# Performance work log

Measured on AMD Instinct MI355X. Metric: run time of the kernel, lower is better.

The kernel has to match this reference:

```python
import jax, jax.numpy as jnp
import numpy as np
from jax import lax

H = 1024  # hidden_size
L = 2     # num_layers


def gru_cell(x, h, Wih, Whh, bih, bhh):
    # PyTorch GRU gate order: r, z, n
    gi = x @ Wih.T + bih          # [B, 3H]
    gh = h @ Whh.T + bhh          # [B, 3H]
    ir, iz, inn = jnp.split(gi, 3, axis=-1)
    hr, hz, hn = jnp.split(gh, 3, axis=-1)
    r = jax.nn.sigmoid(ir + hr)
    z = jax.nn.sigmoid(iz + hz)
    n = jnp.tanh(inn + r * hn)
    return (1.0 - z) * n + z * h


def stacked_step(h, x_t, layers):
    # h: [L, B, H]; x_t: [B, in]; layers: list of (Wih, Whh, bih, bhh)
    hs = []
    inp = x_t
    for l, (Wih, Whh, bih, bhh) in enumerate(layers):
        hl = gru_cell(inp, h[l], Wih, Whh, bih, bhh)
        hs.append(hl)
        inp = hl
    return jnp.stack(hs), inp  # new hidden stack, top-layer output


def run_gru_seq(x_seq, h0, layers):
    # x_seq: [B, S, in] -> scan over time
    def step(h, x_t):
        h_new, out = stacked_step(h, x_t, layers)
        return h_new, out
    h_final, outs = lax.scan(step, h0, jnp.transpose(x_seq, (1, 0, 2)))
    return outs[-1], h_final  # last-timestep top-layer output [B, H]


def setup_inputs() -> dict:
    key = jax.random.key(0)
    ks = jax.random.split(key, 10)
    B, S = 128, 256

    def xavier(k, shape):
        fan_out, fan_in = shape
        std = np.sqrt(2.0 / (fan_in + fan_out))
        return jax.random.normal(k, shape, dtype=jnp.float32) * std

    inp = {
        "x": jax.random.normal(ks[0], (B, S), dtype=jnp.float32),
        "h0": jax.random.uniform(ks[1], (L, B, H), dtype=jnp.float32) * 0.01,
        "Wih0": xavier(ks[2], (3 * H, 1)),
        "Whh0": xavier(ks[3], (3 * H, H)),
        "bih0": jnp.zeros((3 * H,), jnp.float32),
        "bhh0": jnp.zeros((3 * H,), jnp.float32),
        "Wih1": xavier(ks[4], (3 * H, H)),
        "Whh1": xavier(ks[5], (3 * H, H)),
        "bih1": jnp.zeros((3 * H,), jnp.float32),
        "bhh1": jnp.zeros((3 * H,), jnp.float32),
        "fc_w": jax.random.uniform(ks[6], (1, H), jnp.float32, -1.0 / np.sqrt(H), 1.0 / np.sqrt(H)),
        "fc_b": jax.random.uniform(ks[7], (1,), jnp.float32, -1.0 / np.sqrt(H), 1.0 / np.sqrt(H)),
        "forcast_length": 8,
    }
    return inp


def reference(x, h0, Wih0, Whh0, bih0, bhh0, Wih1, Whh1, bih1, bhh1, fc_w, fc_b, forcast_length):
    layers = [(Wih0, Whh0, bih0, bhh0), (Wih1, Whh1, bih1, bhh1)]

    # forecast step i=0: full conditioning sequence
    out0, h = run_gru_seq(x[..., None], h0, layers)   # [B, H], [L, B, H]
    y0 = out0 @ fc_w.T + fc_b                          # [B, 1]

    def fstep(carry, _):
        xc, hc = carry                                 # xc: [B, 1]
        h_new, out = stacked_step(hc, xc, layers)
        y = out @ fc_w.T + fc_b                        # [B, 1]
        return (y, h_new), y[:, 0]

    (y_last, h_final), ys = lax.scan(fstep, (y0, h), None, length=forcast_length - 1)
    forcast_out = jnp.concatenate([y0[:, 0][None, :], ys], axis=0)  # [F, B]
    return jnp.mean(forcast_out, axis=0), h_final
```

## Files before the change

kernel.cpp:

```cpp
#include <hip/hip_runtime.h>

#define NB 128
#define NH 1024
#define NS 256
#define NF 8
#define NBLK 192
#define NTH 512
#define AG  __HIP_MEMORY_SCOPE_AGENT

#define GLOBL 0
#define RELL  64
#define INITL 128
#define XCNT  192
#define XARR  512
#define XCPY  1024

typedef _Float16 half_t;
typedef _Float16 f16x8 __attribute__((ext_vector_type(8)));
typedef float f32x4 __attribute__((ext_vector_type(4)));
typedef unsigned long long u64;

struct GP {
    const float *x, *hin, *Wih0, *Whh0, *bih0, *bhh0, *Wih1, *Whh1, *bih1, *bhh1, *fcw, *fcb;
    float *ypart, *out;
    half_t *h0b0, *h0b1, *h1b0, *h1b1;
    char *reg;
    unsigned *bar;
};

__device__ __forceinline__ float fast_sigmoid(float x) { return 1.0f / (1.0f + __expf(-x)); }
__device__ __forceinline__ float fast_tanh(float x) {
    float e = __expf(2.0f * x);
    return (e - 1.0f) / (e + 1.0f);
}

__device__ __forceinline__ u64 ldu64(const void* p) {
    return __hip_atomic_load((const u64*)p, __ATOMIC_RELAXED, AG);
}
__device__ __forceinline__ void stu64(void* p, u64 v) {
    __hip_atomic_store((u64*)p, v, __ATOMIC_RELAXED, AG);
}
__device__ __forceinline__ float ldf32(const float* p) {
    return __hip_atomic_load(p, __ATOMIC_RELAXED, AG);
}
__device__ __forceinline__ void stf32(float* p, float v) {
    __hip_atomic_store(p, v, __ATOMIC_RELAXED, AG);
}
__device__ __forceinline__ unsigned aadd(unsigned* p, unsigned v) {
    return __hip_atomic_fetch_add(p, v, __ATOMIC_RELAXED, AG);
}
__device__ __forceinline__ unsigned ald(const unsigned* p) {
    return __hip_atomic_load(p, __ATOMIC_RELAXED, AG);
}

__device__ __forceinline__ void l2add(unsigned* p, unsigned v) {
    asm volatile("global_atomic_add %0, %1, off" :: "v"(p), "v"(v) : "memory");
}
__device__ __forceinline__ unsigned l2add_rtn(unsigned* p, unsigned v) {
    unsigned ret;
    asm volatile("global_atomic_add %0, %1, %2, off sc0\n\ts_waitcnt vmcnt(0)"
                 : "=v"(ret) : "v"(p), "v"(v) : "memory");
    return ret;
}

__global__ void k_init(const float* __restrict__ hin, half_t* __restrict__ h0h,
                       half_t* __restrict__ h1h) {
    int i = blockIdx.x * 256 + threadIdx.x;
    h0h[i] = (half_t)hin[i];
    h1h[i] = (half_t)hin[NB * NH + i];
}

__global__ __launch_bounds__(NTH)
void k_gru(GP p) {
    extern __shared__ char lds[];
    const int tid = threadIdx.x;
    const int l   = tid & 63;
    const int wv  = tid >> 6;
    const int bid = blockIdx.x;
    const int role = (bid < 64) ? 0 : 1;
    const int lc   = bid - 64;
    const int colbase = role ? lc * 8 : bid * 16;
    float* hl  = (float*)(lds + 98304);
    int* meta  = (int*)(lds + 106496);
    unsigned* bar = p.bar;

    const int cloc = l & 15;
    const int col8 = cloc & 7;

    {
        for (int i = tid; i < 12288; i += NTH) {
            int row = i >> 8, j = i & 255;
            const float* Wsrc;
            int wrow;
            if (role == 0) {
                Wsrc = p.Whh0; wrow = (row >> 4) * NH + colbase + (row & 15);
            } else {
                int plane = row >> 3, cl = row & 7;
                Wsrc = (plane < 3) ? p.Wih1 : p.Whh1;
                int g = (plane < 3) ? plane : plane - 3;
                wrow = g * NH + colbase + cl;
            }
            float4 v = *(const float4*)(Wsrc + (size_t)wrow * NH + j * 4);
            union { half_t h[4]; uint2 u; } cv;
            cv.h[0] = (half_t)v.x; cv.h[1] = (half_t)v.y;
            cv.h[2] = (half_t)v.z; cv.h[3] = (half_t)v.w;
            *(uint2*)(lds + (row * 2048 + ((j * 8) ^ ((row & 7) << 4)))) = cv.u;
        }
        if (role == 0) {
            for (int i = tid; i < NB * 16; i += NTH)
                hl[i] = p.hin[(size_t)(i >> 4) * NH + colbase + (i & 15)];
        } else {
            for (int i = tid; i < NB * 8; i += NTH)
                hl[i] = p.hin[(size_t)NB * NH + (size_t)(i >> 3) * NH + colbase + (i & 7)];
        }
    }

    if (tid == 0) {
        unsigned x;
        asm volatile("s_getreg_b32 %0, hwreg(HW_REG_XCC_ID)" : "=s"(x));
        x &= 7;
        unsigned r = aadd(bar + XCNT + x * 32, 1u);
        asm volatile("s_waitcnt vmcnt(0)" ::: "memory");
        aadd(bar + INITL, 1u);
        while (ald(bar + INITL) < NBLK) __builtin_amdgcn_s_sleep(1);
        int nn = 0, cnt = 0;
        for (int k = 0; k < 8; ++k) {
            unsigned c = ald(bar + XCNT + k * 32);
            if (c) ++cnt;
            if (k == (int)x) nn = (int)c;
        }
        meta[0] = (int)x; meta[1] = (int)r; meta[2] = nn; meta[3] = cnt;
    }
    __syncthreads();
    const int xcd_  = meta[0];
    const int rank_ = meta[1];
    const int n_    = meta[2];
    const int nx_   = meta[3];

    float bi_[3] = {0,0,0}, bh_[3] = {0,0,0}, wx_[3] = {0,0,0}, fcwv = 0.f, fcb_ = 0.f;
    float bi_lo = 0.f, bh_lo = 0.f, bi2 = 0.f, bh2 = 0.f;
    if (role == 0) {
        int c = colbase + cloc;
        #pragma unroll
        for (int g = 0; g < 3; ++g) {
            bi_[g] = p.bih0[g * NH + c]; bh_[g] = p.bhh0[g * NH + c];
            wx_[g] = p.Wih0[g * NH + c];
        }
        fcb_ = p.fcb[0];
    } else {
        int glo = cloc >> 3;
        int c8 = colbase + col8;
        bi_lo = p.bih1[glo * NH + c8]; bh_lo = p.bhh1[glo * NH + c8];
        bi2   = p.bih1[2 * NH + c8];   bh2   = p.bhh1[2 * NH + c8];
        fcwv  = p.fcw[c8];
    }

    const int rb_l0[3] = { cloc * 2048, (16 + cloc) * 2048, (32 + cloc) * 2048 };
    const int rb_l1[4] = { cloc * 2048, (16 + col8) * 2048, (24 + cloc) * 2048, (40 + col8) * 2048 };
    const int rmask = (col8) << 4;
    const int kb0 = (l >> 4) << 4;
    const int arow = wv * 16 + cloc;
    const int b0base = wv * 16 + ((l >> 4) << 2);
    const int aloff = (l >> 4) * 2048 + arow * 16;

    auto gbar = [&](unsigned t) {
        __syncthreads();
        if (tid == 0) {
            l2add(bar + XARR + xcd_ * 32, 1u);
            if (rank_ == 0) {
                while (l2add_rtn(bar + XARR + xcd_ * 32, 0u) < (unsigned)n_ * t)
                    __builtin_amdgcn_s_sleep(1);
                unsigned old = aadd(bar + GLOBL, 1u);
                if (old == (unsigned)nx_ * t - 1u) aadd(bar + RELL, 1u);
            }
            while (ald(bar + RELL) < t) __builtin_amdgcn_s_sleep(1);
        }
        __syncthreads();
        asm volatile("buffer_inv" ::: "memory");
    };

    auto xcopy = [&](const half_t* h0s, const half_t* h1s, int slot) {
        char* dst = p.reg + ((size_t)(xcd_ * 2 + slot)) * 524288;
        for (int idx = rank_ * NTH + tid; idx < 32768; idx += n_ * NTH) {
            int which = idx >> 14, kq = (idx >> 7) & 127, row = idx & 127;
            const half_t* s = (which ? h1s : h0s) + row * 1024 + kq * 8;
            union { u64 u[2]; uint4 v; } t;
            t.u[0] = ldu64(s);
            t.u[1] = ldu64(s + 4);
            *(uint4*)(dst + which * 262144 + (size_t)(kq * 128 + row) * 16) = t.v;
        }
    };
    auto csync = [&](unsigned ct) {
        __syncthreads();
        if (tid == 0) {
            l2add(bar + XCPY + xcd_ * 32, 1u);
            while (l2add_rtn(bar + XCPY + xcd_ * 32, 0u) < (unsigned)n_ * ct)
                __builtin_amdgcn_s_sleep(1);
        }
        __syncthreads();
    };

    auto gemm_l0 = [&](const char* regA, f32x4 (&acc)[3]) {
        const char* ap = regA + aloff;
        #pragma unroll 8
        for (int ks = 0; ks < 32; ++ks) {
            f16x8 a = *(const f16x8*)(ap + (size_t)ks * 8192);
            int kb = ks * 64 + kb0;
            #pragma unroll
            for (int g = 0; g < 3; ++g) {
                f16x8 bf = *(const f16x8*)(lds + rb_l0[g] + (kb ^ rmask));
                acc[g] = __builtin_amdgcn_mfma_f32_16x16x32_f16(a, bf, acc[g], 0, 0, 0);
            }
        }
    };

    auto gemm_l1 = [&](const char* regA, f32x4 (&acc)[4]) {
        const char* ap0 = regA + aloff;
        const char* ap1 = regA + 262144 + aloff;
        #pragma unroll 8
        for (int ks = 0; ks < 32; ++ks) {
            f16x8 a0 = *(const f16x8*)(ap0 + (size_t)ks * 8192);
            f16x8 a1 = *(const f16x8*)(ap1 + (size_t)ks * 8192);
            int kb = ks * 64 + kb0;
            f16x8 b0 = *(const f16x8*)(lds + rb_l1[0] + (kb ^ rmask));
            acc[0] = __builtin_amdgcn_mfma_f32_16x16x32_f16(a0, b0, acc[0], 0, 0, 0);
            f16x8 b1 = *(const f16x8*)(lds + rb_l1[1] + (kb ^ rmask));
            acc[1] = __builtin_amdgcn_mfma_f32_16x16x32_f16(a0, b1, acc[1], 0, 0, 0);
            f16x8 b2 = *(const f16x8*)(lds + rb_l1[2] + (kb ^ rmask));
            acc[2] = __builtin_amdgcn_mfma_f32_16x16x32_f16(a1, b2, acc[2], 0, 0, 0);
            f16x8 b3 = *(const f16x8*)(lds + rb_l1[3] + (kb ^ rmask));
            acc[3] = __builtin_amdgcn_mfma_f32_16x16x32_f16(a1, b3, acc[3], 0, 0, 0);
        }
    };

    auto pack_store16 = [&](half_t* hw, int b, float hn) {
        unsigned v = (unsigned)__builtin_bit_cast(unsigned short, (half_t)hn);
        unsigned o = __shfl_xor(v, 1);
        unsigned pair = (l & 1) ? (o | (v << 16)) : (v | (o << 16));
        unsigned p2 = __shfl_xor(pair, 2);
        u64 quad = (l & 2) ? (((u64)pair << 32) | p2) : ((u64)pair | ((u64)p2 << 32));
        if ((l & 3) == 0) stu64(hw + (size_t)b * NH + ((colbase + cloc) & ~3), quad);
    };

    auto l0_epi = [&](const float xv[4], f32x4 (&acc)[3], half_t* hw) {
        #pragma unroll
        for (int q = 0; q < 4; ++q) {
            int b = b0base + q;
            float gh0 = acc[0][q] + bh_[0];
            float gh1 = acc[1][q] + bh_[1];
            float gh2 = acc[2][q] + bh_[2];
            float r_ = fast_sigmoid(xv[q] * wx_[0] + bi_[0] + gh0);
            float z_ = fast_sigmoid(xv[q] * wx_[1] + bi_[1] + gh1);
            float n_2 = fast_tanh(xv[q] * wx_[2] + bi_[2] + r_ * gh2);
            float hp = hl[b * 16 + cloc];
            float hn = (1.0f - z_) * n_2 + z_ * hp;
            hl[b * 16 + cloc] = hn;
            pack_store16(hw, b, hn);
        }
    };

    auto l1_epi = [&](f32x4 (&acc)[4], half_t* hw, float* ydst) {
        #pragma unroll
        for (int q = 0; q < 4; ++q) {
            int b = b0base + q;
            float rz = fast_sigmoid(acc[0][q] + bi_lo + acc[2][q] + bh_lo);
            float zv = __shfl_xor(rz, 8);
            float n_2 = fast_tanh(acc[1][q] + bi2 + rz * (acc[3][q] + bh2));
            float hp = hl[b * 8 + col8];
            float hn = (1.0f - zv) * n_2 + zv * hp;
            if (cloc < 8) hl[b * 8 + col8] = hn;
            unsigned v = (unsigned)__builtin_bit_cast(unsigned short, (half_t)hn);
            unsigned o = __shfl_xor(v, 1);
            unsigned pair = (l & 1) ? (o | (v << 16)) : (v | (o << 16));
            unsigned p2 = __shfl_xor(pair, 2);
            u64 quad = (l & 2) ? (((u64)pair << 32) | p2) : ((u64)pair | ((u64)p2 << 32));
            if ((l & 3) == 0 && cloc < 8)
                stu64(hw + (size_t)b * NH + ((colbase + col8) & ~3), quad);
            if (ydst) {
                float s = hn * fcwv;
                s += __shfl_xor(s, 1);
                s += __shfl_xor(s, 2);
                s += __shfl_xor(s, 4);
                if (cloc == 0) stf32(ydst + lc * NB + b, s);
            }
        }
    };

    auto reduce_y = [&](float xv[4]) {
        #pragma unroll
        for (int q = 0; q < 4; ++q) {
            int b = b0base + q;
            float t0 = ldf32(p.ypart + (cloc * 8 + 0) * NB + b);
            float t1 = ldf32(p.ypart + (cloc * 8 + 1) * NB + b);
            float t2 = ldf32(p.ypart + (cloc * 8 + 2) * NB + b);
            float t3 = ldf32(p.ypart + (cloc * 8 + 3) * NB + b);
            float t4 = ldf32(p.ypart + (cloc * 8 + 4) * NB + b);
            float t5 = ldf32(p.ypart + (cloc * 8 + 5) * NB + b);
            float t6 = ldf32(p.ypart + (cloc * 8 + 6) * NB + b);
            float t7 = ldf32(p.ypart + (cloc * 8 + 7) * NB + b);
            xv[q] = ((t0 + t1) + (t2 + t3)) + ((t4 + t5) + (t6 + t7));
        }
        #pragma unroll
        for (int m = 1; m < 16; m <<= 1) {
            xv[0] += __shfl_xor(xv[0], m); xv[1] += __shfl_xor(xv[1], m);
            xv[2] += __shfl_xor(xv[2], m); xv[3] += __shfl_xor(xv[3], m);
        }
        #pragma unroll
        for (int q = 0; q < 4; ++q) xv[q] += fcb_;
    };

    unsigned tgt = 0, ctgt = 0;
    int cur0 = 0, cur1 = 0;
    f32x4 zero4 = {0.f, 0.f, 0.f, 0.f};
    float ysum[4] = {0.f, 0.f, 0.f, 0.f};

    auto COPY = [&]() {
        ++ctgt;
        int slot = (int)(ctgt & 1);
        xcopy(cur0 ? p.h0b1 : p.h0b0, cur1 ? p.h1b1 : p.h1b0, slot);
        csync(ctgt);
        return (const char*)(p.reg + (size_t)(xcd_ * 2 + slot) * 524288);
    };

    for (int ph = 0; ph <= NS; ++ph) {
        float xv[4];
        if (role == 0 && ph < NS) {
            #pragma unroll
            for (int q = 0; q < 4; ++q) xv[q] = p.x[(size_t)(b0base + q) * NS + ph];
        }
        const char* regB = COPY();
        if (role == 0 && ph < NS) {
            f32x4 acc[3] = {zero4, zero4, zero4};
            gemm_l0(regB, acc);
            l0_epi(xv, acc, cur0 ? p.h0b0 : p.h0b1);
        } else if (role == 1 && ph >= 1) {
            f32x4 acc[4] = {zero4, zero4, zero4, zero4};
            gemm_l1(regB, acc);
            l1_epi(acc, cur1 ? p.h1b0 : p.h1b1, (ph == NS) ? p.ypart : nullptr);
        }
        ++tgt; gbar(tgt);
        if (ph < NS) cur0 ^= 1;
        if (ph >= 1) cur1 ^= 1;
    }

    for (int i = 1; i < NF; ++i) {
        float xv[4];
        if (role == 0) {
            reduce_y(xv);
            #pragma unroll
            for (int q = 0; q < 4; ++q) ysum[q] += xv[q];
        }
        const char* regB = COPY();
        if (role == 0) {
            f32x4 acc[3] = {zero4, zero4, zero4};
            gemm_l0(regB, acc);
            l0_epi(xv, acc, cur0 ? p.h0b0 : p.h0b1);
        }
        ++tgt; gbar(tgt); cur0 ^= 1;

        regB = COPY();
        if (role == 1) {
            f32x4 acc[4] = {zero4, zero4, zero4, zero4};
            gemm_l1(regB, acc);
            l1_epi(acc, cur1 ? p.h1b0 : p.h1b1, p.ypart);
        }
        ++tgt; gbar(tgt); cur1 ^= 1;
    }

    if (role == 0) {
        float y7[4];
        reduce_y(y7);
        if (bid == 0 && cloc == 0) {
            #pragma unroll
            for (int q = 0; q < 4; ++q)
                p.out[b0base + q] = (ysum[q] + y7[q]) * 0.125f;
        }
        float* ob = p.out + NB;
        for (int i = tid; i < NB * 16; i += NTH)
            ob[(size_t)(i >> 4) * NH + colbase + (i & 15)] = hl[i];
    } else {
        float* ob = p.out + NB + (size_t)NB * NH;
        for (int i = tid; i < NB * 8; i += NTH)
            ob[(size_t)(i >> 3) * NH + colbase + (i & 7)] = hl[i];
    }
}

extern "C" void kernel_launch(void* const* d_in, const int* in_sizes, int n_in,
                              void* d_out, int out_size, void* d_ws, size_t ws_size,
                              hipStream_t stream)
{
    GP p;
    p.x    = (const float*)d_in[0];
    p.hin  = (const float*)d_in[1];
    p.Wih0 = (const float*)d_in[2];
    p.Whh0 = (const float*)d_in[3];
    p.bih0 = (const float*)d_in[4];
    p.bhh0 = (const float*)d_in[5];
    p.Wih1 = (const float*)d_in[6];
    p.Whh1 = (const float*)d_in[7];
    p.bih1 = (const float*)d_in[8];
    p.bhh1 = (const float*)d_in[9];
    p.fcw  = (const float*)d_in[10];
    p.fcb  = (const float*)d_in[11];
    p.out  = (float*)d_out;

    char* ws = (char*)d_ws;
    p.bar   = (unsigned*)ws;                     ws += 8192;
    p.h0b0  = (half_t*)ws;                       ws += 262144;
    p.h0b1  = (half_t*)ws;                       ws += 262144;
    p.h1b0  = (half_t*)ws;                       ws += 262144;
    p.h1b1  = (half_t*)ws;                       ws += 262144;
    p.ypart = (float*)ws;                        ws += 65536;
    ws = (char*)(((size_t)ws + 4095) & ~(size_t)4095);
    p.reg   = ws;                                ws += 8 * 2 * 524288;

    hipMemsetAsync(p.bar, 0, 8192, stream);
    k_init<<<512, 256, 0, stream>>>(p.hin, p.h0b0, p.h1b0);

    void* args[] = { &p };
    if (hipLaunchCooperativeKernel((void*)k_gru, dim3(NBLK), dim3(NTH), args,
                                   106752, stream) != hipSuccess) {
        (void)hipGetLastError();
        k_gru<<<dim3(NBLK), dim3(NTH), 106752, stream>>>(p);
    }
}
```

Measured before the change: 3.844 ms.

## Split K across wave halves with 2x M-tiling and LDS reduction

Each wave now computes two 16-row M tiles over half of the K dimension, so every B fragment loaded from LDS feeds two MFMAs. The two K halves are combined through a new LDS scratch area, with an extra __syncthreads before the epilogue. This halves the B-operand LDS reads per MFMA and shortens each wave's serial K loop. In exchange it adds a block barrier and a reduction step inside every recurrent step, raises register pressure, and grows dynamic LDS to about 136 KB.

```diff
diff --git a/kernel.cpp b/kernel.cpp
--- a/kernel.cpp
+++ b/kernel.cpp
@@ -76,12 +76,15 @@
     const int tid = threadIdx.x;
     const int l   = tid & 63;
     const int wv  = tid >> 6;
+    const int mh  = wv & 3;
+    const int kh  = wv >> 2;
     const int bid = blockIdx.x;
     const int role = (bid < 64) ? 0 : 1;
     const int lc   = bid - 64;
     const int colbase = role ? lc * 8 : bid * 16;
     float* hl  = (float*)(lds + 98304);
     int* meta  = (int*)(lds + 106496);
+    float* red = (float*)(lds + 106752);
     unsigned* bar = p.bar;
 
     const int cloc = l & 15;
@@ -157,11 +160,10 @@
 
     const int rb_l0[3] = { cloc * 2048, (16 + cloc) * 2048, (32 + cloc) * 2048 };
     const int rb_l1[4] = { cloc * 2048, (16 + col8) * 2048, (24 + cloc) * 2048, (40 + col8) * 2048 };
-    const int rmask = (col8) << 4;
-    const int kb0 = (l >> 4) << 4;
-    const int arow = wv * 16 + cloc;
-    const int b0base = wv * 16 + ((l >> 4) << 2);
-    const int aloff = (l >> 4) * 2048 + arow * 16;
+    const int rmask = col8 << 4;
+    const int kb_base = kh * 1024 + ((l >> 4) << 4);
+    const int b0base = mh * 32 + ((l >> 4) << 2);
+    const int aloff = (kh * 64 + (l >> 4)) * 2048 + (mh * 32 + cloc) * 16;
 
     auto gbar = [&](unsigned t) {
         __syncthreads();
@@ -200,36 +202,44 @@
         __syncthreads();
     };
 
-    auto gemm_l0 = [&](const char* regA, f32x4 (&acc)[3]) {
+    auto gemm_l0 = [&](const char* regA, f32x4 (&acc)[2][3]) {
         const char* ap = regA + aloff;
         #pragma unroll 8
-        for (int ks = 0; ks < 32; ++ks) {
-            f16x8 a = *(const f16x8*)(ap + (size_t)ks * 8192);
-            int kb = ks * 64 + kb0;
+        for (int ks = 0; ks < 16; ++ks) {
+            f16x8 a0 = *(const f16x8*)(ap + ks * 8192);
+            f16x8 a1 = *(const f16x8*)(ap + ks * 8192 + 256);
+            int kb = kb_base + ks * 64;
             #pragma unroll
             for (int g = 0; g < 3; ++g) {
                 f16x8 bf = *(const f16x8*)(lds + rb_l0[g] + (kb ^ rmask));
-                acc[g] = __builtin_amdgcn_mfma_f32_16x16x32_f16(a, bf, acc[g], 0, 0, 0);
-            }
-        }
-    };
-
-    auto gemm_l1 = [&](const char* regA, f32x4 (&acc)[4]) {
+                acc[0][g] = __builtin_amdgcn_mfma_f32_16x16x32_f16(a0, bf, acc[0][g], 0, 0, 0);
+                acc[1][g] = __builtin_amdgcn_mfma_f32_16x16x32_f16(a1, bf, acc[1][g], 0, 0, 0);
+            }
+        }
+    };
+
+    auto gemm_l1 = [&](const char* regA, f32x4 (&acc)[2][4]) {
         const char* ap0 = regA + aloff;
         const char* ap1 = regA + 262144 + aloff;
-        #pragma unroll 8
-        for (int ks = 0; ks < 32; ++ks) {
-            f16x8 a0 = *(const f16x8*)(ap0 + (size_t)ks * 8192);
-            f16x8 a1 = *(const f16x8*)(ap1 + (size_t)ks * 8192);
-            int kb = ks * 64 + kb0;
+        #pragma unroll 4
+        for (int ks = 0; ks < 16; ++ks) {
+            f16x8 a00 = *(const f16x8*)(ap0 + ks * 8192);
+            f16x8 a01 = *(const f16x8*)(ap0 + ks * 8192 + 256);
+            f16x8 a10 = *(const f16x8*)(ap1 + ks * 8192);
+            f16x8 a11 = *(const f16x8*)(ap1 + ks * 8192 + 256);
+            int kb = kb_base + ks * 64;
             f16x8 b0 = *(const f16x8*)(lds + rb_l1[0] + (kb ^ rmask));
-            acc[0] = __builtin_amdgcn_mfma_f32_16x16x32_f16(a0, b0, acc[0], 0, 0, 0);
+            acc[0][0] = __builtin_amdgcn_mfma_f32_16x16x32_f16(a00, b0, acc[0][0], 0, 0, 0);
+            acc[1][0] = __builtin_amdgcn_mfma_f32_16x16x32_f16(a01, b0, acc[1][0], 0, 0, 0);
             f16x8 b1 = *(const f16x8*)(lds + rb_l1[1] + (kb ^ rmask));
-            acc[1] = __builtin_amdgcn_mfma_f32_16x16x32_f16(a0, b1, acc[1], 0, 0, 0);
+            acc[0][1] = __builtin_amdgcn_mfma_f32_16x16x32_f16(a00, b1, acc[0][1], 0, 0, 0);
+            acc[1][1] = __builtin_amdgcn_mfma_f32_16x16x32_f16(a01, b1, acc[1][1], 0, 0, 0);
             f16x8 b2 = *(const f16x8*)(lds + rb_l1[2] + (kb ^ rmask));
-            acc[2] = __builtin_amdgcn_mfma_f32_16x16x32_f16(a1, b2, acc[2], 0, 0, 0);
+            acc[0][2] = __builtin_amdgcn_mfma_f32_16x16x32_f16(a10, b2, acc[0][2], 0, 0, 0);
+            acc[1][2] = __builtin_amdgcn_mfma_f32_16x16x32_f16(a11, b2, acc[1][2], 0, 0, 0);
             f16x8 b3 = *(const f16x8*)(lds + rb_l1[3] + (kb ^ rmask));
-            acc[3] = __builtin_amdgcn_mfma_f32_16x16x32_f16(a1, b3, acc[3], 0, 0, 0);
+            acc[0][3] = __builtin_amdgcn_mfma_f32_16x16x32_f16(a10, b3, acc[0][3], 0, 0, 0);
+            acc[1][3] = __builtin_amdgcn_mfma_f32_16x16x32_f16(a11, b3, acc[1][3], 0, 0, 0);
         }
     };
 
@@ -242,77 +252,78 @@
         if ((l & 3) == 0) stu64(hw + (size_t)b * NH + ((colbase + cloc) & ~3), quad);
     };
 
-    auto l0_epi = [&](const float xv[4], f32x4 (&acc)[3], half_t* hw) {
+    auto l0_epi = [&](const float xv[2][4], f32x4 (&acc)[2][3], half_t* hw) {
         #pragma unroll
-        for (int q = 0; q < 4; ++q) {
-            int b = b0base + q;
-            float gh0 = acc[0][q] + bh_[0];
-            float gh1 = acc[1][q] + bh_[1];
-            float gh2 = acc[2][q] + bh_[2];
-            float r_ = fast_sigmoid(xv[q] * wx_[0] + bi_[0] + gh0);
-            float z_ = fast_sigmoid(xv[q] * wx_[1] + bi_[1] + gh1);
-            float n_2 = fast_tanh(xv[q] * wx_[2] + bi_[2] + r_ * gh2);
-            float hp = hl[b * 16 + cloc];
-            float hn = (1.0f - z_) * n_2 + z_ * hp;
-            hl[b * 16 + cloc] = hn;
-            pack_store16(hw, b, hn);
-        }
-    };
-
-    auto l1_epi = [&](f32x4 (&acc)[4], half_t* hw, float* ydst) {
+        for (int m = 0; m < 2; ++m) {
+            #pragma unroll
+            for (int q = 0; q < 4; ++q) {
+                int b = b0base + m * 16 + q;
+                float gh0 = acc[m][0][q] + bh_[0];
+                float gh1 = acc[m][1][q] + bh_[1];
+                float gh2 = acc[m][2][q] + bh_[2];
+                float r_ = fast_sigmoid(xv[m][q] * wx_[0] + bi_[0] + gh0);
+                float z_ = fast_sigmoid(xv[m][q] * wx_[1] + bi_[1] + gh1);
+                float n_2 = fast_tanh(xv[m][q] * wx_[2] + bi_[2] + r_ * gh2);
+                float hp = hl[b * 16 + cloc];
+                float hn = (1.0f - z_) * n_2 + z_ * hp;
+                hl[b * 16 + cloc] = hn;
+                pack_store16(hw, b, hn);
+            }
+        }
+    };
+
+    auto l1_epi = [&](f32x4 (&acc)[2][4], half_t* hw, float* ydst) {
         #pragma unroll
-        for (int q = 0; q < 4; ++q) {
-            int b = b0base + q;
-            float rz = fast_sigmoid(acc[0][q] + bi_lo + acc[2][q] + bh_lo);
-            float zv = __shfl_xor(rz, 8);
-            float n_2 = fast_tanh(acc[1][q] + bi2 + rz * (acc[3][q] + bh2));
-            float hp = hl[b * 8 + col8];
-            float hn = (1.0f - zv) * n_2 + zv * hp;
-            if (cloc < 8) hl[b * 8 + col8] = hn;
-            unsigned v = (unsigned)__builtin_bit_cast(unsigned short, (half_t)hn);
-            unsigned o = __shfl_xor(v, 1);
-            unsigned pair = (l & 1) ? (o | (v << 16)) : (v | (o << 16));
-            unsigned p2 = __shfl_xor(pair, 2);
-            u64 quad = (l & 2) ? (((u64)pair << 32) | p2) : ((u64)pair | ((u64)p2 << 32));
-            if ((l & 3) == 0 && cloc < 8)
-                stu64(hw + (size_t)b * NH + ((colbase + col8) & ~3), quad);
-            if (ydst) {
-                float s = hn * fcwv;
-                s += __shfl_xor(s, 1);
-                s += __shfl_xor(s, 2);
-                s += __shfl_xor(s, 4);
-                if (cloc == 0) stf32(ydst + lc * NB + b, s);
-            }
-        }
-    };
-
-    auto reduce_y = [&](float xv[4]) {
+        for (int m = 0; m < 2; ++m) {
+            #pragma unroll
+            for (int q = 0; q < 4; ++q) {
+                int b = b0base + m * 16 + q;
+                float rz = fast_sigmoid(acc[m][0][q] + bi_lo + acc[m][2][q] + bh_lo);
+                float zv = __shfl_xor(rz, 8);
+                float n_2 = fast_tanh(acc[m][1][q] + bi2 + rz * (acc[m][3][q] + bh2));
+                float hp = hl[b * 8 + col8];
+                float hn = (1.0f - zv) * n_2 + zv * hp;
+                if (cloc < 8) hl[b * 8 + col8] = hn;
+                unsigned v = (unsigned)__builtin_bit_cast(unsigned short, (half_t)hn);
+                unsigned o = __shfl_xor(v, 1);
+                unsigned pair = (l & 1) ? (o | (v << 16)) : (v | (o << 16));
+                unsigned p2 = __shfl_xor(pair, 2);
+                u64 quad = (l & 2) ? (((u64)pair << 32) | p2) : ((u64)pair | ((u64)p2 << 32));
+                if ((l & 3) == 0 && cloc < 8)
+                    stu64(hw + (size_t)b * NH + ((colbase + col8) & ~3), quad);
+                if (ydst) {
+                    float s = hn * fcwv;
+                    s += __shfl_xor(s, 1);
+                    s += __shfl_xor(s, 2);
+                    s += __shfl_xor(s, 4);
+                    if (cloc == 0) stf32(ydst + lc * NB + b, s);
+                }
+            }
+        }
+    };
+
+    auto reduce_y = [&](float xv[2][4]) {
         #pragma unroll
-        for (int q = 0; q < 4; ++q) {
-            int b = b0base + q;
-            float t0 = ldf32(p.ypart + (cloc * 8 + 0) * NB + b);
-            float t1 = ldf32(p.ypart + (cloc * 8 + 1) * NB + b);
-            float t2 = ldf32(p.ypart + (cloc * 8 + 2) * NB + b);
-            float t3 = ldf32(p.ypart + (cloc * 8 + 3) * NB + b);
-            float t4 = ldf32(p.ypart + (cloc * 8 + 4) * NB + b);
-            float t5 = ldf32(p.ypart + (cloc * 8 + 5) * NB + b);
-            float t6 = ldf32(p.ypart + (cloc * 8 + 6) * NB + b);
-            float t7 = ldf32(p.ypart + (cloc * 8 + 7) * NB + b);
-            xv[q] = ((t0 + t1) + (t2 + t3)) + ((t4 + t5) + (t6 + t7));
-        }
-        #pragma unroll
-        for (int m = 1; m < 16; m <<= 1) {
-            xv[0] += __shfl_xor(xv[0], m); xv[1] += __shfl_xor(xv[1], m);
-            xv[2] += __shfl_xor(xv[2], m); xv[3] += __shfl_xor(xv[3], m);
-        }
-        #pragma unroll
-        for (int q = 0; q < 4; ++q) xv[q] += fcb_;
+        for (int m = 0; m < 2; ++m) {
+            #pragma unroll
+            for (int q = 0; q < 4; ++q) {
+                int b = b0base + m * 16 + q;
+                float t[8];
+                #pragma unroll
+                for (int j = 0; j < 8; ++j)
+                    t[j] = ldf32(p.ypart + (cloc * 8 + j) * NB + b);
+                float s = ((t[0] + t[1]) + (t[2] + t[3])) + ((t[4] + t[5]) + (t[6] + t[7]));
+                #pragma unroll
+                for (int mm = 1; mm < 16; mm <<= 1) s += __shfl_xor(s, mm);
+                xv[m][q] = s + fcb_;
+            }
+        }
     };
 
     unsigned tgt = 0, ctgt = 0;
     int cur0 = 0, cur1 = 0;
     f32x4 zero4 = {0.f, 0.f, 0.f, 0.f};
-    float ysum[4] = {0.f, 0.f, 0.f, 0.f};
+    float ysum[2][4] = {{0.f,0.f,0.f,0.f},{0.f,0.f,0.f,0.f}};
 
     auto COPY = [&]() {
         ++ctgt;
@@ -322,21 +333,62 @@
         return (const char*)(p.reg + (size_t)(xcd_ * 2 + slot) * 524288);
     };
 
+    float* redbase = red + mh * 2048 + (l << 2);
+
     for (int ph = 0; ph <= NS; ++ph) {
-        float xv[4];
-        if (role == 0 && ph < NS) {
-            #pragma unroll
-            for (int q = 0; q < 4; ++q) xv[q] = p.x[(size_t)(b0base + q) * NS + ph];
+        float xv[2][4];
+        if (role == 0 && ph < NS && kh == 0) {
+            #pragma unroll
+            for (int m = 0; m < 2; ++m)
+                #pragma unroll
+                for (int q = 0; q < 4; ++q)
+                    xv[m][q] = p.x[(size_t)(b0base + m * 16 + q) * NS + ph];
         }
         const char* regB = COPY();
         if (role == 0 && ph < NS) {
-            f32x4 acc[3] = {zero4, zero4, zero4};
+            f32x4 acc[2][3];
+            #pragma unroll
+            for (int m = 0; m < 2; ++m) { acc[m][0] = zero4; acc[m][1] = zero4; acc[m][2] = zero4; }
             gemm_l0(regB, acc);
-            l0_epi(xv, acc, cur0 ? p.h0b0 : p.h0b1);
+            if (kh == 1) {
+                #pragma unroll
+                for (int m = 0; m < 2; ++m)
+                    #pragma unroll
+                    for (int g = 0; g < 3; ++g)
+                        *(f32x4*)(redbase + (m * 3 + g) * 256) = acc[m][g];
+            }
+            __syncthreads();
+            if (kh == 0) {
+                #pragma unroll
+                for (int m = 0; m < 2; ++m)
+                    #pragma unroll
+                    for (int g = 0; g < 3; ++g)
+                        acc[m][g] += *(const f32x4*)(redbase + (m * 3 + g) * 256);
+                l0_epi(xv, acc, cur0 ? p.h0b0 : p.h0b1);
+            }
         } else if (role == 1 && ph >= 1) {
-            f32x4 acc[4] = {zero4, zero4, zero4, zero4};
+            f32x4 acc[2][4];
+            #pragma unroll
+            for (int m = 0; m < 2; ++m)
+                #pragma unroll
+                for (int g = 0; g < 4; ++g) acc[m][g] = zero4;
             gemm_l1(regB, acc);
-            l1_epi(acc, cur1 ? p.h1b0 : p.h1b1, (ph == NS) ? p.ypart : nullptr);
+            if (kh == 1) {
+                #pragma unroll
+                for (int m = 0; m < 2; ++m)
+                    #pragma unroll
+                    for (int g = 0; g < 4; ++g)
+                        *(f32x4*)(redbase + (m * 4 + g) * 256) = acc[m][g];
+            }
+            __syncthreads();
+            if (kh == 0) {
+                #pragma unroll
+                for (int m = 0; m < 2; ++m)
+                    #pragma unroll
+                    for (int g = 0; g < 4; ++g)
+                        acc[m][g] += *(const f32x4*)(redbase + (m * 4 + g) * 256);
+                l1_epi(acc, cur1 ? p.h1b0 : p.h1b1, (ph == NS) ? p.ypart : nullptr);
+            }
         }
         ++tgt; gbar(tgt);
         if (ph < NS) cur0 ^= 1;
@@ -344,37 +396,79 @@
     }
 
     for (int i = 1; i < NF; ++i) {
-        float xv[4];
-        if (role == 0) {
+        float xv[2][4];
+        if (role == 0 && kh == 0) {
             reduce_y(xv);
             #pragma unroll
-            for (int q = 0; q < 4; ++q) ysum[q] += xv[q];
+            for (int m = 0; m < 2; ++m)
+                #pragma unroll
+                for (int q = 0; q < 4; ++q) ysum[m][q] += xv[m][q];
         }
         const char* regB = COPY();
         if (role == 0) {
-            f32x4 acc[3] = {zero4, zero4, zero4};
+            f32x4 acc[2][3];
+            #pragma unroll
+            for (int m = 0; m < 2; ++m) { acc[m][0] = zero4; acc[m][1] = zero4; acc[m][2] = zero4; }
             gemm_l0(regB, acc);
-            l0_epi(xv, acc, cur0 ? p.h0b0 : p.h0b1);
+            if (kh == 1) {
+                #pragma unroll
+                for (int m = 0; m < 2; ++m)
+                    #pragma unroll
+                    for (int g = 0; g < 3; ++g)
+                        *(f32x4*)(redbase + (m * 3 + g) * 256) = acc[m][g];
+            }
+            __syncthreads();
+            if (kh == 0) {
+                #pragma unroll
+                for (int m = 0; m < 2; ++m)
+                    #pragma unroll
+                    for (int g = 0; g < 3; ++g)
+                        acc[m][g] += *(const f32x4*)(redbase + (m * 3 + g) * 256);
+                l0_epi(xv, acc, cur0 ? p.h0b0 : p.h0b1);
+            }
         }
         ++tgt; gbar(tgt); cur0 ^= 1;
 
         regB = COPY();
         if (role == 1) {
-            f32x4 acc[4] = {zero4, zero4, zero4, zero4};
+            f32x4 acc[2][4];
+            #pragma unroll
+            for (int m = 0; m < 2; ++m)
+                #pragma unroll
+                for (int g = 0; g < 4; ++g) acc[m][g] = zero4;
             gemm_l1(regB, acc);
-            l1_epi(acc, cur1 ? p.h1b0 : p.h1b1, p.ypart);
+            if (kh == 1) {
+                #pragma unroll
+                for (int m = 0; m < 2; ++m)
+                    #pragma unroll
+                    for (int g = 0; g < 4; ++g)
+                        *(f32x4*)(redbase + (m * 4 + g) * 256) = acc[m][g];
+            }
+            __syncthreads();
+            if (kh == 0) {
+                #pragma unroll
+                for (int m = 0; m < 2; ++m)
+                    #pragma unroll
+                    for (int g = 0; g < 4; ++g)
+                        acc[m][g] += *(const f32x4*)(redbase + (m * 4 + g) * 256);
+                l1_epi(acc, cur1 ? p.h1b0 : p.h1b1, p.ypart);
+            }
         }
         ++tgt; gbar(tgt); cur1 ^= 1;
     }
 
-    if (role == 0) {
-        float y7[4];
+    if (role == 0 && kh == 0) {
+        float y7[2][4];
         reduce_y(y7);
         if (bid == 0 && cloc == 0) {
             #pragma unroll
-            for (int q = 0; q < 4; ++q)
-                p.out[b0base + q] = (ysum[q] + y7[q]) * 0.125f;
-        }
+            for (int m = 0; m < 2; ++m)
+                #pragma unroll
+                for (int q = 0; q < 4; ++q)
+                    p.out[b0base + m * 16 + q] = (ysum[m][q] + y7[m][q]) * 0.125f;
+        }
+    }
+    if (role == 0) {
         float* ob = p.out + NB;
         for (int i = tid; i < NB * 16; i += NTH)
             ob[(size_t)(i >> 4) * NH + colbase + (i & 15)] = hl[i];
@@ -419,8 +513,8 @@
 
     void* args[] = { &p };
     if (hipLaunchCooperativeKernel((void*)k_gru, dim3(NBLK), dim3(NTH), args,
-                                   106752, stream) != hipSuccess) {
+                                   139520, stream) != hipSuccess) {
         (void)hipGetLastError();
-        k_gru<<<dim3(NBLK), dim3(NTH), 106752, stream>>>(p);
-    }
-}
+        k_gru<<<dim3(NBLK), dim3(NTH), 139520, stream>>>(p);
+    }
+}
```

Result: faster. 3.501 ms (-8.9%).
